# Performance work log

Measured on AMD Instinct MI355X. Metric: run time of the kernel, lower is better.

Reference implementation:

```python
import jax, jax.numpy as jnp
import numpy as np

B, NQ, NK, D = 8, 2048, 2048, 1024

def setup_inputs() -> dict:
    key = jax.random.key(0)
    k1, k2, k3, k4, k5 = jax.random.split(key, 5)
    query_input = jax.random.normal(k1, (B, NQ, D), dtype=jnp.float32)
    key_input = jax.random.normal(k2, (B, NK, D), dtype=jnp.float32)
    s = 1.0 / np.sqrt(D)
    # nn.Linear(in,out,bias=False): y = x @ W.T, W shape (out,in)
    Wq = jax.random.uniform(k3, (D, D), dtype=jnp.float32, minval=-s, maxval=s)
    Wk = jax.random.uniform(k4, (D, D), dtype=jnp.float32, minval=-s, maxval=s)
    Wv = jax.random.uniform(k5, (D, D), dtype=jnp.float32, minval=-s, maxval=s)
    return {"query_input": query_input, "key_input": key_input,
            "Wq": Wq, "Wk": Wk, "Wv": Wv}

def reference(query_input, key_input, Wq, Wk, Wv):
    d = query_input.shape[-1]
    q = jnp.einsum('bnd,ed->bne', query_input, Wq)   # (b, n_q, d)
    k = jnp.einsum('bmd,ed->bme', key_input, Wk)     # (b, n_k, d)
    v = jnp.einsum('bnd,ed->bne', query_input, Wv)   # (b, n_q, d) -- value from query_input
    # scores: K @ Q^T -> (b, n_k, n_q), softmax over n_q
    a = jnp.einsum('bmd,bnd->bmn', k, q) / jnp.sqrt(jnp.float32(d))
    a = jax.nn.softmax(a, axis=-1)
    context = jnp.einsum('bmn,bnd->bmd', a, v)       # (b, n_k, d)
    return context + key_input
```

## Files before the change

kernel.cpp:

```cpp
#include <hip/hip_runtime.h>
#include <hip/hip_bf16.h>

using bf16 = __bf16;
typedef __bf16 bf16x8 __attribute__((ext_vector_type(8)));
typedef float f32x4 __attribute__((ext_vector_type(4)));

__device__ __forceinline__ void gload_lds16(const bf16* g, bf16* l) {
  __builtin_amdgcn_global_load_lds(
      (const __attribute__((address_space(1))) void*)g,
      (__attribute__((address_space(3))) void*)l, 16, 0, 0);
}

__global__ __launch_bounds__(256) void cvt_f32_bf16(const float* __restrict__ in,
                                                    bf16* __restrict__ out, int n) {
  int i = (blockIdx.x * 256 + threadIdx.x) * 8;
  if (i >= n) return;
  float4 f0 = *(const float4*)&in[i];
  float4 f1 = *(const float4*)&in[i + 4];
  bf16x8 o;
  o[0] = (bf16)f0.x; o[1] = (bf16)f0.y; o[2] = (bf16)f0.z; o[3] = (bf16)f0.w;
  o[4] = (bf16)f1.x; o[5] = (bf16)f1.y; o[6] = (bf16)f1.z; o[7] = (bf16)f1.w;
  *(bf16x8*)&out[i] = o;
}

template <int EPI>
__global__ __launch_bounds__(512, 2)
void gemm_bt(const bf16* __restrict__ A, const bf16* __restrict__ B,
             void* __restrict__ Cv, const float* __restrict__ Add,
             const float* __restrict__ Inv,
             int K, int lda, int ldb, int ldc,
             long sA, long sB, long sC, long sAdd, float scale) {
  int bx = blockIdx.x, by = blockIdx.y, bz = blockIdx.z;
  if (gridDim.z > 1) {
    const int gx = gridDim.x, gxy = gx * gridDim.y;
    const int nwg = gxy * gridDim.z;
    int lin = bx + gx * by + gxy * bz;
    lin = (lin & 7) * (nwg >> 3) + (lin >> 3);
    bz = lin / gxy; const int rem = lin - bz * gxy;
    by = rem / gx;  bx = rem - by * gx;
  }
  A += (long)bz * sA;
  B += (long)bz * sB;
  const int tid = threadIdx.x;
  const int lane = tid & 63;
  const int wave = tid >> 6;
  const int wr = wave >> 2;
  const int wc = wave & 3;
  const long brow = (long)bx * 256;
  const long bcol = (long)by * 256;

  __shared__ bf16 lds[4][16384];

  f32x4 acc[8][4] = {};

  const int srow = tid >> 2;
  const int scg  = (tid & 3) ^ ((srow >> 1) & 3);
  const bf16* gA = A + (brow + srow) * (long)lda + scg * 8;
  const bf16* gB = B + (bcol + srow) * (long)ldb + scg * 8;
  const long a128 = (long)lda << 7;
  const long b128 = (long)ldb << 7;

  const int nk = K >> 5;

  auto stageAlo = [&](int t) { gload_lds16(gA + (long)t * 32,        lds[t & 3] + tid * 8); };
  auto stageAhi = [&](int t) { gload_lds16(gA + a128 + (long)t * 32, lds[t & 3] + 4096 + tid * 8); };
  auto stageBlo = [&](int t) { gload_lds16(gB + (long)t * 32,        lds[t & 3] + 8192 + tid * 8); };
  auto stageBhi = [&](int t) { gload_lds16(gB + b128 + (long)t * 32, lds[t & 3] + 12288 + tid * 8); };

  stageAlo(0); stageAhi(0); stageBlo(0); stageBhi(0);
  stageAlo(1); stageAhi(1); stageBlo(1); stageBhi(1);
  stageAlo(2); stageAhi(2); stageBlo(2); stageBhi(2);
  asm volatile("s_waitcnt vmcnt(8)" ::: "memory");
  __builtin_amdgcn_s_barrier();

  const int lk = lane >> 4;
  const int lr = lane & 15;

  auto rdA = [&](const bf16* buf, int mi) -> bf16x8 {
    const int r = wr * 128 + mi * 16 + lr;
    return *(const bf16x8*)&buf[r * 32 + ((lk ^ ((r >> 1) & 3)) << 3)];
  };
  auto rdB = [&](const bf16* buf, int ni) -> bf16x8 {
    const int r = wc * 64 + ni * 16 + lr;
    return *(const bf16x8*)&buf[8192 + r * 32 + ((lk ^ ((r >> 1) & 3)) << 3)];
  };

  for (int t = 0; t < nk; ++t) {
    bf16* buf = lds[t & 3];
    bf16x8 av[8], bv[4];
#pragma unroll
    for (int mi = 0; mi < 4; ++mi) av[mi] = rdA(buf, mi);
#pragma unroll
    for (int ni = 0; ni < 2; ++ni) bv[ni] = rdB(buf, ni);
    if (t + 3 < nk) stageAlo(t + 3);
    __builtin_amdgcn_s_barrier();
    asm volatile("s_waitcnt lgkmcnt(0)" ::: "memory");
    __builtin_amdgcn_sched_barrier(0);
    __builtin_amdgcn_s_setprio(1);
#pragma unroll
    for (int mi = 0; mi < 4; ++mi)
#pragma unroll
      for (int ni = 0; ni < 2; ++ni)
        acc[mi][ni] = __builtin_amdgcn_mfma_f32_16x16x32_bf16(av[mi], bv[ni], acc[mi][ni], 0, 0, 0);
    __builtin_amdgcn_s_setprio(0);
    __builtin_amdgcn_s_barrier();
#pragma unroll
    for (int ni = 2; ni < 4; ++ni) bv[ni] = rdB(buf, ni);
    if (t + 3 < nk) stageAhi(t + 3);
    __builtin_amdgcn_s_barrier();
    asm volatile("s_waitcnt lgkmcnt(0)" ::: "memory");
    __builtin_amdgcn_sched_barrier(0);
    __builtin_amdgcn_s_setprio(1);
#pragma unroll
    for (int mi = 0; mi < 4; ++mi)
#pragma unroll
      for (int ni = 2; ni < 4; ++ni)
        acc[mi][ni] = __builtin_amdgcn_mfma_f32_16x16x32_bf16(av[mi], bv[ni], acc[mi][ni], 0, 0, 0);
    __builtin_amdgcn_s_setprio(0);
    __builtin_amdgcn_s_barrier();
#pragma unroll
    for (int mi = 4; mi < 8; ++mi) av[mi] = rdA(buf, mi);
    if (t + 3 < nk) stageBlo(t + 3);
    __builtin_amdgcn_s_barrier();
    asm volatile("s_waitcnt lgkmcnt(0)" ::: "memory");
    __builtin_amdgcn_sched_barrier(0);
    __builtin_amdgcn_s_setprio(1);
#pragma unroll
    for (int mi = 4; mi < 8; ++mi)
#pragma unroll
      for (int ni = 2; ni < 4; ++ni)
        acc[mi][ni] = __builtin_amdgcn_mfma_f32_16x16x32_bf16(av[mi], bv[ni], acc[mi][ni], 0, 0, 0);
    __builtin_amdgcn_s_setprio(0);
    __builtin_amdgcn_s_barrier();
    if (t + 3 < nk) stageBhi(t + 3);
    __builtin_amdgcn_s_barrier();
    __builtin_amdgcn_s_setprio(1);
#pragma unroll
    for (int mi = 4; mi < 8; ++mi)
#pragma unroll
      for (int ni = 0; ni < 2; ++ni)
        acc[mi][ni] = __builtin_amdgcn_mfma_f32_16x16x32_bf16(av[mi], bv[ni], acc[mi][ni], 0, 0, 0);
    __builtin_amdgcn_s_setprio(0);
    if (t < nk - 3)       { asm volatile("s_waitcnt vmcnt(8)" ::: "memory"); }
    else if (t == nk - 3) { asm volatile("s_waitcnt vmcnt(4)" ::: "memory"); }
    else if (t == nk - 2) { asm volatile("s_waitcnt vmcnt(0)" ::: "memory"); }
    __builtin_amdgcn_s_barrier();
  }

  const int or0 = wr * 128 + ((lane >> 4) << 2);
  const int oc0 = wc * 64 + (lane & 15);
#pragma unroll
  for (int mi = 0; mi < 8; ++mi) {
#pragma unroll
    for (int ni = 0; ni < 4; ++ni) {
#pragma unroll
      for (int j = 0; j < 4; ++j) {
        const long row = brow + or0 + mi * 16 + j;
        const long col = bcol + oc0 + ni * 16;
        if constexpr (EPI == 0) {
          bf16* C = (bf16*)Cv + (long)bz * sC;
          C[row * ldc + col] = (bf16)(acc[mi][ni][j] * scale);
        } else if constexpr (EPI == 1) {
          bf16* C = (bf16*)Cv + (long)bz * sC;
          C[row * ldc + col] = (bf16)__expf(acc[mi][ni][j] * scale);
        } else {
          float* C = (float*)Cv + (long)bz * sC;
          const float* Ad = Add + (long)bz * sAdd;
          const float* iv = Inv + (long)bz * 2048;
          C[row * ldc + col] = acc[mi][ni][j] * iv[row] + Ad[row * ldc + col];
        }
      }
    }
  }
}

__global__ __launch_bounds__(256) void rowsum_inv(const bf16* __restrict__ E,
                                                  float* __restrict__ inv) {
  const long row = blockIdx.x;
  const bf16* p = E + row * 2048;
  const int tid = threadIdx.x;
  bf16x8 v = *(const bf16x8*)&p[tid * 8];
  float s = 0.f;
#pragma unroll
  for (int i = 0; i < 8; ++i) s += (float)v[i];
#pragma unroll
  for (int off = 32; off > 0; off >>= 1) s += __shfl_xor(s, off, 64);
  __shared__ float red[4];
  if ((tid & 63) == 0) red[tid >> 6] = s;
  __syncthreads();
  if (tid == 0) inv[row] = 1.0f / (red[0] + red[1] + red[2] + red[3]);
}

extern "C" void kernel_launch(void* const* d_in, const int* in_sizes, int n_in,
                              void* d_out, int out_size, void* d_ws, size_t ws_size,
                              hipStream_t stream) {
  const float* q_in = (const float*)d_in[0];
  const float* k_in = (const float*)d_in[1];
  const float* Wq   = (const float*)d_in[2];
  const float* Wk   = (const float*)d_in[3];
  const float* Wv   = (const float*)d_in[4];
  float* out = (float*)d_out;
  char* ws = (char*)d_ws;

  bf16* qb  = (bf16*)(ws);
  bf16* kb  = (bf16*)(ws + 33554432);
  bf16* S   = (bf16*)(ws);
  bf16* Wqb = (bf16*)(ws + 67108864);
  float* inv = (float*)(ws + 67108864);
  bf16* Wkb = (bf16*)(ws + 69206016);
  bf16* Wvb = (bf16*)(ws + 71303168);
  bf16* Qp  = (bf16*)(ws + 73400320);
  bf16* Kp  = (bf16*)(ws + 106954752);
  bf16* Vpt = (bf16*)(ws + 140509184);

  cvt_f32_bf16<<<8192, 256, 0, stream>>>(q_in, qb, 16777216);
  cvt_f32_bf16<<<8192, 256, 0, stream>>>(k_in, kb, 16777216);
  cvt_f32_bf16<<<512, 256, 0, stream>>>(Wq, Wqb, 1048576);
  cvt_f32_bf16<<<512, 256, 0, stream>>>(Wk, Wkb, 1048576);
  cvt_f32_bf16<<<512, 256, 0, stream>>>(Wv, Wvb, 1048576);

  gemm_bt<0><<<dim3(64, 4, 1), 512, 0, stream>>>(
      qb, Wqb, Qp, nullptr, nullptr, 1024, 1024, 1024, 1024, 0, 0, 0, 0, 1.0f);
  gemm_bt<0><<<dim3(64, 4, 1), 512, 0, stream>>>(
      kb, Wkb, Kp, nullptr, nullptr, 1024, 1024, 1024, 1024, 0, 0, 0, 0, 1.0f);
  gemm_bt<0><<<dim3(4, 8, 8), 512, 0, stream>>>(
      Wvb, qb, Vpt, nullptr, nullptr, 1024, 1024, 1024, 2048,
      0L, 2097152L, 2097152L, 0L, 1.0f);

  gemm_bt<1><<<dim3(8, 8, 8), 512, 0, stream>>>(
      Kp, Qp, S, nullptr, nullptr, 1024, 1024, 1024, 2048,
      2097152L, 2097152L, 4194304L, 0L, 0.03125f);

  rowsum_inv<<<16384, 256, 0, stream>>>(S, inv);

  gemm_bt<2><<<dim3(8, 4, 8), 512, 0, stream>>>(
      S, Vpt, out, k_in, inv, 2048, 2048, 2048, 1024,
      4194304L, 2097152L, 2097152L, 2097152L, 1.0f);
}
```

Baseline: 341.9 us.

## Deepen GEMM K-step to 64 with double-buffered LDS and staggered prefetch

Restructures the bf16 GEMM main loop from a 4-stage ring of 32-wide K tiles to a 2-stage double buffer of 64-wide K tiles, with a new 8-way XOR swizzle for the 128-byte rows. Each phase now issues twice as many MFMAs per barrier, halving the loop-iteration and barrier count, and loads are staggered across the phases of the previous tile. The cost is shallower prefetch depth (one tile ahead instead of three), more operand registers held live, and more complex vmcnt accounting.

```diff
diff --git a/kernel.cpp b/kernel.cpp
--- a/kernel.cpp
+++ b/kernel.cpp
@@ -49,101 +49,119 @@
   const long brow = (long)bx * 256;
   const long bcol = (long)by * 256;
 
-  __shared__ bf16 lds[4][16384];
+  __shared__ bf16 lds[65536];
 
   f32x4 acc[8][4] = {};
 
-  const int srow = tid >> 2;
-  const int scg  = (tid & 3) ^ ((srow >> 1) & 3);
-  const bf16* gA = A + (brow + srow) * (long)lda + scg * 8;
-  const bf16* gB = B + (bcol + srow) * (long)ldb + scg * 8;
-  const long a128 = (long)lda << 7;
-  const long b128 = (long)ldb << 7;
-
-  const int nk = K >> 5;
-
-  auto stageAlo = [&](int t) { gload_lds16(gA + (long)t * 32,        lds[t & 3] + tid * 8); };
-  auto stageAhi = [&](int t) { gload_lds16(gA + a128 + (long)t * 32, lds[t & 3] + 4096 + tid * 8); };
-  auto stageBlo = [&](int t) { gload_lds16(gB + (long)t * 32,        lds[t & 3] + 8192 + tid * 8); };
-  auto stageBhi = [&](int t) { gload_lds16(gB + b128 + (long)t * 32, lds[t & 3] + 12288 + tid * 8); };
-
-  stageAlo(0); stageAhi(0); stageBlo(0); stageBhi(0);
-  stageAlo(1); stageAhi(1); stageBlo(1); stageBhi(1);
-  stageAlo(2); stageAhi(2); stageBlo(2); stageBhi(2);
-  asm volatile("s_waitcnt vmcnt(8)" ::: "memory");
-  __builtin_amdgcn_s_barrier();
+  const int srow = tid >> 3;
+  const int scs  = (tid & 7) ^ (srow & 7);
+  const bf16* gA = A + (brow + srow) * (long)lda + scs * 8;
+  const bf16* gB = B + (bcol + srow) * (long)ldb + scs * 8;
+
+  const int nk = K >> 6;
+
+  auto stageA = [&](int t, int h) {
+    bf16* dst = lds + (t & 1) * 32768 + h * 8192 + tid * 8;
+    const bf16* g = gA + ((long)h * 128) * lda + (long)t * 64;
+    gload_lds16(g, dst);
+    gload_lds16(g + (long)64 * lda, dst + 4096);
+  };
+  auto stageB = [&](int t, int h) {
+    bf16* dst = lds + (t & 1) * 32768 + 16384 + h * 8192 + tid * 8;
+    const bf16* g = gB + ((long)h * 128) * ldb + (long)t * 64;
+    gload_lds16(g, dst);
+    gload_lds16(g + (long)64 * ldb, dst + 4096);
+  };
 
   const int lk = lane >> 4;
   const int lr = lane & 15;
 
-  auto rdA = [&](const bf16* buf, int mi) -> bf16x8 {
-    const int r = wr * 128 + mi * 16 + lr;
-    return *(const bf16x8*)&buf[r * 32 + ((lk ^ ((r >> 1) & 3)) << 3)];
-  };
-  auto rdB = [&](const bf16* buf, int ni) -> bf16x8 {
-    const int r = wc * 64 + ni * 16 + lr;
-    return *(const bf16x8*)&buf[8192 + r * 32 + ((lk ^ ((r >> 1) & 3)) << 3)];
-  };
+  auto rdA = [&](int d, int mi, int ks) -> bf16x8 {
+    const int rt = wr * 128 + mi * 16 + lr;
+    const int h = rt >> 7, r = rt & 127;
+    const int c = (ks * 4 + lk) ^ (r & 7);
+    return *(const bf16x8*)&lds[d * 32768 + h * 8192 + r * 64 + c * 8];
+  };
+  auto rdB = [&](int d, int ni, int ks) -> bf16x8 {
+    const int rt = wc * 64 + ni * 16 + lr;
+    const int h = rt >> 7, r = rt & 127;
+    const int c = (ks * 4 + lk) ^ (r & 7);
+    return *(const bf16x8*)&lds[d * 32768 + 16384 + h * 8192 + r * 64 + c * 8];
+  };
+
+  stageA(0, 0); stageA(0, 1); stageB(0, 0); stageB(0, 1);
+  stageA(1, 0);
+  asm volatile("s_waitcnt vmcnt(2)" ::: "memory");
+  __builtin_amdgcn_s_barrier();
+
+  bf16x8 av[8][2], bv[4][2];
 
   for (int t = 0; t < nk; ++t) {
-    bf16* buf = lds[t & 3];
-    bf16x8 av[8], bv[4];
-#pragma unroll
-    for (int mi = 0; mi < 4; ++mi) av[mi] = rdA(buf, mi);
-#pragma unroll
-    for (int ni = 0; ni < 2; ++ni) bv[ni] = rdB(buf, ni);
-    if (t + 3 < nk) stageAlo(t + 3);
+    const int d = t & 1;
+#pragma unroll
+    for (int mi = 0; mi < 4; ++mi) { av[mi][0] = rdA(d, mi, 0); av[mi][1] = rdA(d, mi, 1); }
+#pragma unroll
+    for (int ni = 0; ni < 2; ++ni) { bv[ni][0] = rdB(d, ni, 0); bv[ni][1] = rdB(d, ni, 1); }
+    if (t + 1 < nk) stageA(t + 1, 1);
+    asm volatile("s_waitcnt lgkmcnt(8)" ::: "memory");
     __builtin_amdgcn_s_barrier();
     asm volatile("s_waitcnt lgkmcnt(0)" ::: "memory");
     __builtin_amdgcn_sched_barrier(0);
     __builtin_amdgcn_s_setprio(1);
 #pragma unroll
-    for (int mi = 0; mi < 4; ++mi)
-#pragma unroll
-      for (int ni = 0; ni < 2; ++ni)
-        acc[mi][ni] = __builtin_amdgcn_mfma_f32_16x16x32_bf16(av[mi], bv[ni], acc[mi][ni], 0, 0, 0);
-    __builtin_amdgcn_s_setprio(0);
-    __builtin_amdgcn_s_barrier();
-#pragma unroll
-    for (int ni = 2; ni < 4; ++ni) bv[ni] = rdB(buf, ni);
-    if (t + 3 < nk) stageAhi(t + 3);
+    for (int ks = 0; ks < 2; ++ks)
+#pragma unroll
+      for (int mi = 0; mi < 4; ++mi)
+#pragma unroll
+        for (int ni = 0; ni < 2; ++ni)
+          acc[mi][ni] = __builtin_amdgcn_mfma_f32_16x16x32_bf16(av[mi][ks], bv[ni][ks], acc[mi][ni], 0, 0, 0);
+    __builtin_amdgcn_s_setprio(0);
+    __builtin_amdgcn_s_barrier();
+#pragma unroll
+    for (int ni = 2; ni < 4; ++ni) { bv[ni][0] = rdB(d, ni, 0); bv[ni][1] = rdB(d, ni, 1); }
+    if (t + 1 < nk) stageB(t + 1, 0);
     __builtin_amdgcn_s_barrier();
     asm volatile("s_waitcnt lgkmcnt(0)" ::: "memory");
     __builtin_amdgcn_sched_barrier(0);
     __builtin_amdgcn_s_setprio(1);
 #pragma unroll
-    for (int mi = 0; mi < 4; ++mi)
-#pragma unroll
-      for (int ni = 2; ni < 4; ++ni)
-        acc[mi][ni] = __builtin_amdgcn_mfma_f32_16x16x32_bf16(av[mi], bv[ni], acc[mi][ni], 0, 0, 0);
-    __builtin_amdgcn_s_setprio(0);
-    __builtin_amdgcn_s_barrier();
-#pragma unroll
-    for (int mi = 4; mi < 8; ++mi) av[mi] = rdA(buf, mi);
-    if (t + 3 < nk) stageBlo(t + 3);
+    for (int ks = 0; ks < 2; ++ks)
+#pragma unroll
+      for (int mi = 0; mi < 4; ++mi)
+#pragma unroll
+        for (int ni = 2; ni < 4; ++ni)
+          acc[mi][ni] = __builtin_amdgcn_mfma_f32_16x16x32_bf16(av[mi][ks], bv[ni][ks], acc[mi][ni], 0, 0, 0);
+    __builtin_amdgcn_s_setprio(0);
+    __builtin_amdgcn_s_barrier();
+#pragma unroll
+    for (int mi = 4; mi < 8; ++mi) { av[mi][0] = rdA(d, mi, 0); av[mi][1] = rdA(d, mi, 1); }
+    if (t + 1 < nk) stageB(t + 1, 1);
     __builtin_amdgcn_s_barrier();
     asm volatile("s_waitcnt lgkmcnt(0)" ::: "memory");
     __builtin_amdgcn_sched_barrier(0);
     __builtin_amdgcn_s_setprio(1);
 #pragma unroll
-    for (int mi = 4; mi < 8; ++mi)
-#pragma unroll
-      for (int ni = 2; ni < 4; ++ni)
-        acc[mi][ni] = __builtin_amdgcn_mfma_f32_16x16x32_bf16(av[mi], bv[ni], acc[mi][ni], 0, 0, 0);
-    __builtin_amdgcn_s_setprio(0);
-    __builtin_amdgcn_s_barrier();
-    if (t + 3 < nk) stageBhi(t + 3);
-    __builtin_amdgcn_s_barrier();
-    __builtin_amdgcn_s_setprio(1);
-#pragma unroll
-    for (int mi = 4; mi < 8; ++mi)
-#pragma unroll
-      for (int ni = 0; ni < 2; ++ni)
-        acc[mi][ni] = __builtin_amdgcn_mfma_f32_16x16x32_bf16(av[mi], bv[ni], acc[mi][ni], 0, 0, 0);
-    __builtin_amdgcn_s_setprio(0);
-    if (t < nk - 3)       { asm volatile("s_waitcnt vmcnt(8)" ::: "memory"); }
-    else if (t == nk - 3) { asm volatile("s_waitcnt vmcnt(4)" ::: "memory"); }
-    else if (t == nk - 2) { asm volatile("s_waitcnt vmcnt(0)" ::: "memory"); }
+    for (int ks = 0; ks < 2; ++ks)
+#pragma unroll
+      for (int mi = 4; mi < 8; ++mi)
+#pragma unroll
+        for (int ni = 2; ni < 4; ++ni)
+          acc[mi][ni] = __builtin_amdgcn_mfma_f32_16x16x32_bf16(av[mi][ks], bv[ni][ks], acc[mi][ni], 0, 0, 0);
+    __builtin_amdgcn_s_setprio(0);
+    __builtin_amdgcn_s_barrier();
+    if (t + 2 < nk) stageA(t + 2, 0);
+    __builtin_amdgcn_s_barrier();
+    __builtin_amdgcn_s_setprio(1);
+#pragma unroll
+    for (int ks = 0; ks < 2; ++ks)
+#pragma unroll
+      for (int mi = 4; mi < 8; ++mi)
+#pragma unroll
+        for (int ni = 0; ni < 2; ++ni)
+          acc[mi][ni] = __builtin_amdgcn_mfma_f32_16x16x32_bf16(av[mi][ks], bv[ni][ks], acc[mi][ni], 0, 0, 0);
+    __builtin_amdgcn_s_setprio(0);
+    if (t + 2 < nk) { asm volatile("s_waitcnt vmcnt(2)" ::: "memory"); }
+    else            { asm volatile("s_waitcnt vmcnt(0)" ::: "memory"); }
     __builtin_amdgcn_s_barrier();
   }
 
```

New measurement: 321.8 us. 5.9% less time.

## Restructure GEMM main loop into register double-buffered fragment prefetch

Applied to the files above, without the earlier changes.

Replaces the four-phase interleaved per-tile schedule (many barriers and partial LDS reads) with a loop unrolled by two that ping-pongs between two full register fragment sets. The LDS reads for the next K-tile overlap the MFMAs of the current one, and each step issues one full-tile global-to-LDS stage and uses one barrier. This is meant to cut barrier and lgkmcnt stalls, at the cost of more VGPRs (24 bf16x8 fragments) under launch_bounds(512,2). The lgkmcnt(12) wait and the buffer-reuse ordering are delicate and could race or spill.

```diff
diff --git a/kernel.cpp b/kernel.cpp
--- a/kernel.cpp
+++ b/kernel.cpp
@@ -21,6 +21,31 @@
   o[0] = (bf16)f0.x; o[1] = (bf16)f0.y; o[2] = (bf16)f0.z; o[3] = (bf16)f0.w;
   o[4] = (bf16)f1.x; o[5] = (bf16)f1.y; o[6] = (bf16)f1.z; o[7] = (bf16)f1.w;
   *(bf16x8*)&out[i] = o;
+}
+
+__device__ __forceinline__ void load_frags(const bf16* __restrict__ buf,
+                                           int wr, int wc, int lk, int lr,
+                                           bf16x8 (&R)[12]) {
+#pragma unroll
+  for (int mi = 0; mi < 8; ++mi) {
+    const int r = wr * 128 + mi * 16 + lr;
+    R[mi] = *(const bf16x8*)&buf[r * 32 + ((lk ^ ((r >> 1) & 3)) << 3)];
+  }
+#pragma unroll
+  for (int ni = 0; ni < 4; ++ni) {
+    const int r = wc * 64 + ni * 16 + lr;
+    R[8 + ni] = *(const bf16x8*)&buf[8192 + r * 32 + ((lk ^ ((r >> 1) & 3)) << 3)];
+  }
+}
+
+__device__ __forceinline__ void mfma_tile(const bf16x8 (&R)[12], f32x4 (&acc)[8][4]) {
+  __builtin_amdgcn_s_setprio(1);
+#pragma unroll
+  for (int mi = 0; mi < 8; ++mi)
+#pragma unroll
+    for (int ni = 0; ni < 4; ++ni)
+      acc[mi][ni] = __builtin_amdgcn_mfma_f32_16x16x32_bf16(R[mi], R[8 + ni], acc[mi][ni], 0, 0, 0);
+  __builtin_amdgcn_s_setprio(0);
 }
 
 template <int EPI>
@@ -62,88 +87,45 @@
 
   const int nk = K >> 5;
 
-  auto stageAlo = [&](int t) { gload_lds16(gA + (long)t * 32,        lds[t & 3] + tid * 8); };
-  auto stageAhi = [&](int t) { gload_lds16(gA + a128 + (long)t * 32, lds[t & 3] + 4096 + tid * 8); };
-  auto stageBlo = [&](int t) { gload_lds16(gB + (long)t * 32,        lds[t & 3] + 8192 + tid * 8); };
-  auto stageBhi = [&](int t) { gload_lds16(gB + b128 + (long)t * 32, lds[t & 3] + 12288 + tid * 8); };
-
-  stageAlo(0); stageAhi(0); stageBlo(0); stageBhi(0);
-  stageAlo(1); stageAhi(1); stageBlo(1); stageBhi(1);
-  stageAlo(2); stageAhi(2); stageBlo(2); stageBhi(2);
-  asm volatile("s_waitcnt vmcnt(8)" ::: "memory");
-  __builtin_amdgcn_s_barrier();
+  auto stage = [&](int t) {
+    bf16* buf = (bf16*)lds[t & 3];
+    const bf16* a = gA + (long)t * 32;
+    const bf16* b = gB + (long)t * 32;
+    gload_lds16(a,        buf + tid * 8);
+    gload_lds16(a + a128, buf + 4096 + tid * 8);
+    gload_lds16(b,        buf + 8192 + tid * 8);
+    gload_lds16(b + b128, buf + 12288 + tid * 8);
+  };
 
   const int lk = lane >> 4;
   const int lr = lane & 15;
 
-  auto rdA = [&](const bf16* buf, int mi) -> bf16x8 {
-    const int r = wr * 128 + mi * 16 + lr;
-    return *(const bf16x8*)&buf[r * 32 + ((lk ^ ((r >> 1) & 3)) << 3)];
-  };
-  auto rdB = [&](const bf16* buf, int ni) -> bf16x8 {
-    const int r = wc * 64 + ni * 16 + lr;
-    return *(const bf16x8*)&buf[8192 + r * 32 + ((lk ^ ((r >> 1) & 3)) << 3)];
-  };
-
-  for (int t = 0; t < nk; ++t) {
-    bf16* buf = lds[t & 3];
-    bf16x8 av[8], bv[4];
-#pragma unroll
-    for (int mi = 0; mi < 4; ++mi) av[mi] = rdA(buf, mi);
-#pragma unroll
-    for (int ni = 0; ni < 2; ++ni) bv[ni] = rdB(buf, ni);
-    if (t + 3 < nk) stageAlo(t + 3);
+  stage(0); stage(1); stage(2);
+  asm volatile("s_waitcnt vmcnt(4)" ::: "memory");
+  __builtin_amdgcn_s_barrier();
+
+  bf16x8 R0[12], R1[12];
+  load_frags((const bf16*)lds[0], wr, wc, lk, lr, R0);
+
+  for (int t = 0; t < nk; t += 2) {
+    load_frags((const bf16*)lds[(t + 1) & 3], wr, wc, lk, lr, R1);
+    if (t + 3 < nk) stage(t + 3);
+    __builtin_amdgcn_sched_barrier(0);
+    asm volatile("s_waitcnt lgkmcnt(12)" ::: "memory");
+    __builtin_amdgcn_sched_barrier(0);
+    mfma_tile(R0, acc);
+    if (t + 3 < nk) { asm volatile("s_waitcnt vmcnt(4)" ::: "memory"); }
+    else            { asm volatile("s_waitcnt vmcnt(0)" ::: "memory"); }
     __builtin_amdgcn_s_barrier();
-    asm volatile("s_waitcnt lgkmcnt(0)" ::: "memory");
-    __builtin_amdgcn_sched_barrier(0);
-    __builtin_amdgcn_s_setprio(1);
-#pragma unroll
-    for (int mi = 0; mi < 4; ++mi)
-#pragma unroll
-      for (int ni = 0; ni < 2; ++ni)
-        acc[mi][ni] = __builtin_amdgcn_mfma_f32_16x16x32_bf16(av[mi], bv[ni], acc[mi][ni], 0, 0, 0);
-    __builtin_amdgcn_s_setprio(0);
-    __builtin_amdgcn_s_barrier();
-#pragma unroll
-    for (int ni = 2; ni < 4; ++ni) bv[ni] = rdB(buf, ni);
-    if (t + 3 < nk) stageAhi(t + 3);
-    __builtin_amdgcn_s_barrier();
-    asm volatile("s_waitcnt lgkmcnt(0)" ::: "memory");
-    __builtin_amdgcn_sched_barrier(0);
-    __builtin_amdgcn_s_setprio(1);
-#pragma unroll
-    for (int mi = 0; mi < 4; ++mi)
-#pragma unroll
-      for (int ni = 2; ni < 4; ++ni)
-        acc[mi][ni] = __builtin_amdgcn_mfma_f32_16x16x32_bf16(av[mi], bv[ni], acc[mi][ni], 0, 0, 0);
-    __builtin_amdgcn_s_setprio(0);
-    __builtin_amdgcn_s_barrier();
-#pragma unroll
-    for (int mi = 4; mi < 8; ++mi) av[mi] = rdA(buf, mi);
-    if (t + 3 < nk) stageBlo(t + 3);
-    __builtin_amdgcn_s_barrier();
-    asm volatile("s_waitcnt lgkmcnt(0)" ::: "memory");
-    __builtin_amdgcn_sched_barrier(0);
-    __builtin_amdgcn_s_setprio(1);
-#pragma unroll
-    for (int mi = 4; mi < 8; ++mi)
-#pragma unroll
-      for (int ni = 2; ni < 4; ++ni)
-        acc[mi][ni] = __builtin_amdgcn_mfma_f32_16x16x32_bf16(av[mi], bv[ni], acc[mi][ni], 0, 0, 0);
-    __builtin_amdgcn_s_setprio(0);
-    __builtin_amdgcn_s_barrier();
-    if (t + 3 < nk) stageBhi(t + 3);
-    __builtin_amdgcn_s_barrier();
-    __builtin_amdgcn_s_setprio(1);
-#pragma unroll
-    for (int mi = 4; mi < 8; ++mi)
-#pragma unroll
-      for (int ni = 0; ni < 2; ++ni)
-        acc[mi][ni] = __builtin_amdgcn_mfma_f32_16x16x32_bf16(av[mi], bv[ni], acc[mi][ni], 0, 0, 0);
-    __builtin_amdgcn_s_setprio(0);
-    if (t < nk - 3)       { asm volatile("s_waitcnt vmcnt(8)" ::: "memory"); }
-    else if (t == nk - 3) { asm volatile("s_waitcnt vmcnt(4)" ::: "memory"); }
-    else if (t == nk - 2) { asm volatile("s_waitcnt vmcnt(0)" ::: "memory"); }
+    if (t + 2 < nk) load_frags((const bf16*)lds[(t + 2) & 3], wr, wc, lk, lr, R0);
+    if (t + 4 < nk) stage(t + 4);
+    __builtin_amdgcn_sched_barrier(0);
+    if (t + 2 < nk) { asm volatile("s_waitcnt lgkmcnt(12)" ::: "memory"); }
+    else            { asm volatile("s_waitcnt lgkmcnt(0)" ::: "memory"); }
+    __builtin_amdgcn_sched_barrier(0);
+    mfma_tile(R1, acc);
+    if (t + 4 < nk) { asm volatile("s_waitcnt vmcnt(4)" ::: "memory"); }
+    else            { asm volatile("s_waitcnt vmcnt(0)" ::: "memory"); }
     __builtin_amdgcn_s_barrier();
   }
 
```

Result: faster. 314.4 us (-8.1%).
